# Optimization experiments

Hardware: AMD Instinct MI355X
Metric: run time of the kernel (lower is better)

## Reference

```python
import jax, jax.numpy as jnp
import numpy as np

N = 8192      # number of graph nodes
C = 256       # feature_size
D = C // 2    # projection dim


def setup_inputs() -> dict:
    key = jax.random.key(0)
    ks = jax.random.split(key, 10)
    s_in = 1.0 / np.sqrt(C + 3)   # torch Linear default init scale (uniform bound)
    s_r = 1.0 / np.sqrt(D)
    return {
        "landmarks": jax.random.normal(ks[0], (1, N, 3), dtype=jnp.float32),
        "features": jax.random.normal(ks[1], (1, N, C), dtype=jnp.float32),
        # weights stored [in, out]
        "Wi": jax.random.uniform(ks[2], (C + 3, D), jnp.float32, -s_in, s_in),
        "bi": jax.random.uniform(ks[3], (D,), jnp.float32, -s_in, s_in),
        "Wj": jax.random.uniform(ks[4], (C + 3, D), jnp.float32, -s_in, s_in),
        "bj": jax.random.uniform(ks[5], (D,), jnp.float32, -s_in, s_in),
        "Wk": jax.random.uniform(ks[6], (C + 3, D), jnp.float32, -s_in, s_in),
        "bk": jax.random.uniform(ks[7], (D,), jnp.float32, -s_in, s_in),
        "Wr": jax.random.uniform(ks[8], (D, C), jnp.float32, -s_r, s_r),
        "br": jax.random.uniform(ks[9], (C,), jnp.float32, -s_r, s_r),
    }


def reference(landmarks, features, Wi, bi, Wj, bj, Wk, bk, Wr, br):
    # concat coords + features, drop the singleton batch dim: [N, C+3]
    x = jnp.concatenate([landmarks, features], axis=2)[0]
    fi = x @ Wi + bi                       # [N, D]
    fj = x @ Wj + bj                       # [N, D]
    fk = x @ Wk + bk                       # [N, D]
    att = jax.nn.sigmoid(fi @ fj.T)        # [N, N] sigmoid scores (non-softmax)
    att = att / jnp.sum(att, axis=1, keepdims=True)  # row-sum normalize
    out = (att @ fk) @ Wr + br             # [N, C] restored
    return features + out[None]            # residual, back to [1, N, C]
```

## Files before the change

kernel.cpp:

```cpp
#include <hip/hip_runtime.h>
#include <stdint.h>

#define N_NODES 8192
#define KPAD 272
#define OUTC 384

typedef __attribute__((ext_vector_type(8))) short bhalf8;
typedef __attribute__((ext_vector_type(16))) float f32x16;
typedef __attribute__((ext_vector_type(4))) float f32x4;

__device__ inline unsigned short f2bf_rne(float f) {
    unsigned u = __builtin_bit_cast(unsigned, f);
    u += 0x7FFFu + ((u >> 16) & 1u);
    return (unsigned short)(u >> 16);
}

__device__ inline float bf2f(unsigned short u) {
    return __builtin_bit_cast(float, ((unsigned)u) << 16);
}

__device__ inline bhalf8 mk8(unsigned a, unsigned b, unsigned c, unsigned d) {
    union { unsigned u[4]; bhalf8 v; } U;
    U.u[0] = a; U.u[1] = b; U.u[2] = c; U.u[3] = d;
    return U.v;
}

#define GLD_TO_LDS(gptr, lptr)                                                              \
    __builtin_amdgcn_global_load_lds((const __attribute__((address_space(1))) void*)(gptr), \
                                     (__attribute__((address_space(3))) void*)(lptr), 16, 0, 0)

__global__ void k_prep(const float* __restrict__ landmarks, const float* __restrict__ features,
                       const float* __restrict__ Wi, const float* __restrict__ bi,
                       const float* __restrict__ Wj, const float* __restrict__ bj,
                       const float* __restrict__ Wk, const float* __restrict__ bk,
                       const float* __restrict__ Wr,
                       unsigned short* __restrict__ xb, unsigned short* __restrict__ WcatT,
                       unsigned short* __restrict__ WrT, float* __restrict__ bcat) {
    int idx = blockIdx.x * 256 + threadIdx.x;
    const int XB_N = N_NODES * KPAD;
    const int WC_N = OUTC * KPAD;
    const int WR_N = 256 * 128;
    if (idx < XB_N) {
        int i = idx / KPAD, kk = idx - i * KPAD;
        float v = 0.f;
        if (kk < 256) v = features[i * 256 + kk];
        else if (kk < 259) v = landmarks[i * 3 + (kk - 256)];
        xb[idx] = f2bf_rne(v);
        return;
    }
    idx -= XB_N;
    if (idx < WC_N) {
        int n = idx / KPAD, kk = idx - n * KPAD;
        int sel = n >> 7, d = n & 127;
        const float* W = (sel == 0) ? Wi : ((sel == 1) ? Wj : Wk);
        float v = 0.f;
        if (kk < 256) v = W[(kk + 3) * 128 + d];
        else if (kk < 259) v = W[(kk - 256) * 128 + d];
        WcatT[idx] = f2bf_rne(v);
        return;
    }
    idx -= WC_N;
    if (idx < WR_N) {
        int c = idx >> 7, d = idx & 127;
        WrT[idx] = f2bf_rne(Wr[d * 256 + c]);
        return;
    }
    idx -= WR_N;
    if (idx < OUTC) {
        float v = (idx < 128) ? bi[idx] : ((idx < 256) ? bj[idx - 128] : bk[idx - 256]);
        bcat[idx] = v;
    }
}

__global__ __launch_bounds__(256) void k_proj(const unsigned short* __restrict__ xb,
                                              const unsigned short* __restrict__ WcatT,
                                              const float* __restrict__ bcat,
                                              unsigned short* __restrict__ fi,
                                              unsigned short* __restrict__ fj,
                                              unsigned short* __restrict__ fkT) {
    const int tid = threadIdx.x;
    const int w = tid >> 6, l = tid & 63, h = l >> 5, ln = l & 31;
    const int i0 = blockIdx.x * 32;
    f32x16 acc[3] = {};
#pragma unroll
    for (int s = 0; s < 17; ++s) {
        bhalf8 a = *(const bhalf8*)(xb + (size_t)(i0 + ln) * KPAD + s * 16 + h * 8);
#pragma unroll
        for (int t = 0; t < 3; ++t) {
            int n = 96 * w + 32 * t + ln;
            bhalf8 b = *(const bhalf8*)(WcatT + (size_t)n * KPAD + s * 16 + h * 8);
            acc[t] = __builtin_amdgcn_mfma_f32_32x32x16_bf16(a, b, acc[t], 0, 0, 0);
        }
    }
#pragma unroll
    for (int t = 0; t < 3; ++t) {
        int n = 96 * w + 32 * t + ln;
        int sel = n >> 7, d = n & 127;
        float bias = bcat[n];
#pragma unroll
        for (int q = 0; q < 4; ++q) {
            int ib = i0 + 8 * q + 4 * h;
            if (sel < 2) {
                unsigned short* dst = sel ? fj : fi;
#pragma unroll
                for (int r = 0; r < 4; ++r)
                    dst[(size_t)(ib + r) * 128 + d] = f2bf_rne(acc[t][4 * q + r] + bias);
            } else {
                ushort4 pk;
                pk.x = f2bf_rne(acc[t][4 * q + 0] + bias);
                pk.y = f2bf_rne(acc[t][4 * q + 1] + bias);
                pk.z = f2bf_rne(acc[t][4 * q + 2] + bias);
                pk.w = f2bf_rne(acc[t][4 * q + 3] + bias);
                *(ushort4*)(fkT + (size_t)d * N_NODES + ib) = pk;
            }
        }
    }
}

__global__ __launch_bounds__(256, 2) void k_attn(const unsigned short* __restrict__ fi,
                                                 const unsigned short* __restrict__ fj,
                                                 const unsigned short* __restrict__ fkT,
                                                 unsigned short* __restrict__ num_part,
                                                 float* __restrict__ den_part) {
    __shared__ __align__(16) char smem[66560];
    float* bufA = (float*)smem;
    float* bufB = (float*)(smem + 17408);
    float* denb = (float*)(smem + 65536);

    const int tid = threadIdx.x;
    const int w = tid >> 6, l = tid & 63, h = l >> 5, ln = l & 31;
    const int jq = blockIdx.x & 3, rt = blockIdx.x >> 2;
    const int i0 = rt * 64;
    const int jbase = jq * 2048;

    bhalf8 bfi[2][8];
#pragma unroll
    for (int nt = 0; nt < 2; ++nt)
#pragma unroll
        for (int s = 0; s < 8; ++s)
            bfi[nt][s] = *(const bhalf8*)(fi + (size_t)(i0 + nt * 32 + ln) * 128 + s * 16 + h * 8);

    f32x16 acc[8] = {};
    float dacc0 = 0.f, dacc1 = 0.f;

    const int rsub = l >> 4;
    const int cph = l & 15;

    {
        const int j00 = jbase + ((rt & 15) * 128);
#pragma unroll
        for (int q = 0; q < 8; ++q) {
            int r = w * 32 + q * 4 + rsub;
            int c = cph ^ (r & 15);
            GLD_TO_LDS(fkT + (size_t)r * N_NODES + j00 + c * 8, smem + (w * 32 + q * 4) * 256);
        }
    }

    for (int mt = 0; mt < 16; ++mt) {
        __syncthreads();
        char* fk_cur = smem + ((mt & 1) ? 32768 : 0);
        char* fk_nxt = smem + ((mt & 1) ? 0 : 32768);
        if (mt < 15) {
            const int j0n = jbase + (((mt + 1 + rt) & 15) * 128);
#pragma unroll
            for (int q = 0; q < 8; ++q) {
                int r = w * 32 + q * 4 + rsub;
                int c = cph ^ (r & 15);
                GLD_TO_LDS(fkT + (size_t)r * N_NODES + j0n + c * 8, fk_nxt + (w * 32 + q * 4) * 256);
            }
        }
        const int j0 = jbase + (((mt + rt) & 15) * 128);

        f32x16 st0 = {}, st1 = {};
        const int jrow = j0 + w * 32 + ln;
#pragma unroll
        for (int s = 0; s < 8; ++s) {
            bhalf8 af = *(const bhalf8*)(fj + (size_t)jrow * 128 + s * 16 + h * 8);
            st0 = __builtin_amdgcn_mfma_f32_32x32x16_bf16(af, bfi[0][s], st0, 0, 0, 0);
            st1 = __builtin_amdgcn_mfma_f32_32x32x16_bf16(af, bfi[1][s], st1, 0, 0, 0);
        }

        float sv0[16], sv1[16];
#pragma unroll
        for (int r = 0; r < 16; ++r) {
            float x0 = __builtin_amdgcn_rcpf(1.f + __builtin_amdgcn_exp2f(st0[r] * -1.44269504f));
            float x1 = __builtin_amdgcn_rcpf(1.f + __builtin_amdgcn_exp2f(st1[r] * -1.44269504f));
            dacc0 += x0; dacc1 += x1;
            sv0[r] = x0; sv1[r] = x1;
        }
        unsigned p0[8], p1[8], x0v[8], x1v[8];
#pragma unroll
        for (int q = 0; q < 8; ++q) {
            p0[q] = __builtin_amdgcn_perm(__builtin_bit_cast(unsigned, sv0[2 * q + 1]),
                                          __builtin_bit_cast(unsigned, sv0[2 * q]), 0x07060302u);
            p1[q] = __builtin_amdgcn_perm(__builtin_bit_cast(unsigned, sv1[2 * q + 1]),
                                          __builtin_bit_cast(unsigned, sv1[2 * q]), 0x07060302u);
        }
#pragma unroll
        for (int q = 0; q < 8; ++q) {
            x0v[q] = (unsigned)__shfl_xor((int)p0[q], 32, 64);
            x1v[q] = (unsigned)__shfl_xor((int)p1[q], 32, 64);
        }
        bhalf8 fb[2][2];
        if (h == 0) {
            fb[0][0] = mk8(p0[0], p0[1], x0v[0], x0v[1]);
            fb[0][1] = mk8(p0[4], p0[5], x0v[4], x0v[5]);
            fb[1][0] = mk8(p1[0], p1[1], x1v[0], x1v[1]);
            fb[1][1] = mk8(p1[4], p1[5], x1v[4], x1v[5]);
        } else {
            fb[0][0] = mk8(x0v[2], x0v[3], p0[2], p0[3]);
            fb[0][1] = mk8(x0v[6], x0v[7], p0[6], p0[7]);
            fb[1][0] = mk8(x1v[2], x1v[3], p1[2], p1[3]);
            fb[1][1] = mk8(x1v[6], x1v[7], p1[6], p1[7]);
        }
#pragma unroll
        for (int m4 = 0; m4 < 4; ++m4) {
#pragma unroll
            for (int s2 = 0; s2 < 2; ++s2) {
                int row = m4 * 32 + ln;
                int c = (w * 4 + s2 * 2 + h) ^ (row & 15);
                bhalf8 af = *(const bhalf8*)(fk_cur + row * 256 + c * 16);
                acc[m4 * 2 + 0] = __builtin_amdgcn_mfma_f32_32x32x16_bf16(af, fb[0][s2], acc[m4 * 2 + 0], 0, 0, 0);
                acc[m4 * 2 + 1] = __builtin_amdgcn_mfma_f32_32x32x16_bf16(af, fb[1][s2], acc[m4 * 2 + 1], 0, 0, 0);
            }
        }
    }

    {
        float o0 = __shfl_xor(dacc0, 32, 64);
        float o1 = __shfl_xor(dacc1, 32, 64);
        dacc0 += o0; dacc1 += o1;
    }
    if (h == 0) {
        denb[w * 64 + ln] = dacc0;
        denb[w * 64 + 32 + ln] = dacc1;
    }

#pragma unroll
    for (int half = 0; half < 2; ++half) {
        __syncthreads();
        if (w < 2) {
            float* buf = w ? bufB : bufA;
#pragma unroll
            for (int m2 = 0; m2 < 2; ++m2) {
                int m4 = half * 2 + m2;
#pragma unroll
                for (int nt = 0; nt < 2; ++nt) {
                    int iloc = nt * 32 + ln;
#pragma unroll
                    for (int q = 0; q < 4; ++q) {
                        int d = m2 * 32 + 8 * q + 4 * h;
                        f32x4 v = {acc[m4 * 2 + nt][4 * q + 0], acc[m4 * 2 + nt][4 * q + 1],
                                   acc[m4 * 2 + nt][4 * q + 2], acc[m4 * 2 + nt][4 * q + 3]};
                        *(f32x4*)(buf + iloc * 68 + d) = v;
                    }
                }
            }
        }
        __syncthreads();
        if (w >= 2) {
            float* buf = (w == 3) ? bufB : bufA;
#pragma unroll
            for (int m2 = 0; m2 < 2; ++m2) {
                int m4 = half * 2 + m2;
#pragma unroll
                for (int nt = 0; nt < 2; ++nt) {
                    int iloc = nt * 32 + ln;
#pragma unroll
                    for (int q = 0; q < 4; ++q) {
                        int d = m2 * 32 + 8 * q + 4 * h;
                        f32x4 old = *(f32x4*)(buf + iloc * 68 + d);
                        f32x4 v = {acc[m4 * 2 + nt][4 * q + 0], acc[m4 * 2 + nt][4 * q + 1],
                                   acc[m4 * 2 + nt][4 * q + 2], acc[m4 * 2 + nt][4 * q + 3]};
                        *(f32x4*)(buf + iloc * 68 + d) = old + v;
                    }
                }
            }
        }
        __syncthreads();
#pragma unroll
        for (int e = 0; e < 4; ++e) {
            int v = e * 256 + tid;
            int iloc = v >> 4;
            int d4 = (v & 15) * 4;
            f32x4 s = *(f32x4*)(bufA + iloc * 68 + d4) + *(f32x4*)(bufB + iloc * 68 + d4);
            ushort4 pk;
            pk.x = f2bf_rne(s.x); pk.y = f2bf_rne(s.y);
            pk.z = f2bf_rne(s.z); pk.w = f2bf_rne(s.w);
            *(ushort4*)(num_part + (size_t)(jq * N_NODES + i0 + iloc) * 128 + half * 64 + d4) = pk;
        }
    }
    __syncthreads();
    if (tid < 64) {
        den_part[(size_t)jq * N_NODES + i0 + tid] =
            denb[tid] + denb[64 + tid] + denb[128 + tid] + denb[192 + tid];
    }
}

__global__ __launch_bounds__(256) void k_out(const unsigned short* __restrict__ num_part,
                                             const float* __restrict__ den_part,
                                             const unsigned short* __restrict__ WrT,
                                             const float* __restrict__ br,
                                             const float* __restrict__ features,
                                             float* __restrict__ out) {
    __shared__ __align__(16) char smem[73728];
    unsigned short* t_s = (unsigned short*)(smem + 65536);
    const int tid = threadIdx.x, w = tid >> 6, l = tid & 63, h = l >> 5, ln = l & 31;
    const int i0 = blockIdx.x * 32;
    {
        int rsub = l >> 4, cph = l & 15;
#pragma unroll
        for (int q = 0; q < 16; ++q) {
            int r = w * 64 + q * 4 + rsub;
            int c = cph ^ (r & 15);
            GLD_TO_LDS(WrT + (size_t)r * 128 + c * 8, (char*)smem + (w * 64 + q * 4) * 256);
        }
    }
#pragma unroll
    for (int e = 0; e < 2; ++e) {
        int v = e * 256 + tid;
        int r = v >> 4, c8 = v & 15;
        float s[8] = {};
        float den = 0.f;
#pragma unroll
        for (int q = 0; q < 4; ++q) {
            const unsigned short* p = num_part + (size_t)(q * N_NODES + i0 + r) * 128 + c8 * 8;
            union { uint4 u; unsigned short us[8]; } U;
            U.u = *(const uint4*)p;
#pragma unroll
            for (int z = 0; z < 8; ++z) s[z] += bf2f(U.us[z]);
            den += den_part[(size_t)q * N_NODES + i0 + r];
        }
        float inv = 1.0f / den;
        union { ushort4 a[2]; uint4 u; } P;
#pragma unroll
        for (int z = 0; z < 8; ++z) ((unsigned short*)&P)[z] = f2bf_rne(s[z] * inv);
        int pc = c8 ^ (r & 15);
        *(uint4*)((char*)t_s + r * 256 + pc * 16) = P.u;
    }
    __syncthreads();
    f32x16 acc[2] = {};
#pragma unroll
    for (int s = 0; s < 8; ++s) {
        int ca = (s * 2 + h) ^ (ln & 15);
        bhalf8 af = *(const bhalf8*)((char*)t_s + ln * 256 + ca * 16);
#pragma unroll
        for (int nt = 0; nt < 2; ++nt) {
            int row = w * 64 + nt * 32 + ln;
            int c = (s * 2 + h) ^ (row & 15);
            bhalf8 bf = *(const bhalf8*)((char*)smem + row * 256 + c * 16);
            acc[nt] = __builtin_amdgcn_mfma_f32_32x32x16_bf16(af, bf, acc[nt], 0, 0, 0);
        }
    }
#pragma unroll
    for (int nt = 0; nt < 2; ++nt) {
        int cc = w * 64 + nt * 32 + ln;
        float bias = br[cc];
#pragma unroll
        for (int q = 0; q < 4; ++q) {
#pragma unroll
            for (int r = 0; r < 4; ++r) {
                int i = i0 + 8 * q + 4 * h + r;
                out[(size_t)i * 256 + cc] = acc[nt][4 * q + r] + bias + features[(size_t)i * 256 + cc];
            }
        }
    }
}

extern "C" void kernel_launch(void* const* d_in, const int* in_sizes, int n_in,
                              void* d_out, int out_size, void* d_ws, size_t ws_size,
                              hipStream_t stream) {
    const float* landmarks = (const float*)d_in[0];
    const float* features  = (const float*)d_in[1];
    const float* Wi = (const float*)d_in[2];
    const float* bi = (const float*)d_in[3];
    const float* Wj = (const float*)d_in[4];
    const float* bj = (const float*)d_in[5];
    const float* Wk = (const float*)d_in[6];
    const float* bk = (const float*)d_in[7];
    const float* Wr = (const float*)d_in[8];
    const float* br = (const float*)d_in[9];

    char* ws = (char*)d_ws;
    unsigned short* xb      = (unsigned short*)(ws + 0);
    unsigned short* WcatT   = (unsigned short*)(ws + 4456448);
    unsigned short* WrT     = (unsigned short*)(ws + 4665344);
    float*          bcat    = (float*)(ws + 4730880);
    unsigned short* fi      = (unsigned short*)(ws + 4732416);
    unsigned short* fjp     = (unsigned short*)(ws + 6829568);
    unsigned short* fkT     = (unsigned short*)(ws + 8926720);
    unsigned short* num_part= (unsigned short*)(ws + 11023872);
    float*          den_part= (float*)(ws + 19412480);

    float* out = (float*)d_out;

    hipLaunchKernelGGL(k_prep, dim3(9242), dim3(256), 0, stream,
                       landmarks, features, Wi, bi, Wj, bj, Wk, bk, Wr, xb, WcatT, WrT, bcat);
    hipLaunchKernelGGL(k_proj, dim3(256), dim3(256), 0, stream, xb, WcatT, bcat, fi, fjp, fkT);
    hipLaunchKernelGGL(k_attn, dim3(512), dim3(256), 0, stream, fi, fjp, fkT, num_part, den_part);
    hipLaunchKernelGGL(k_out, dim3(256), dim3(256), 0, stream, num_part, den_part, WrT, br, features, out);
}
```

Before: 183.2 us.

## Restage attention fi into LDS, prefetch fj into registers, and widen proj/out grids

The attention kernel now stages fi through LDS instead of holding it in registers. It double-buffers the fj rows in registers, prefetching the next tile's fj alongside the fk LDS staging, and unrolls the loop by two tiles so the global fj loads overlap with compute. The projection and output kernels are split across more blocks (three output segments and two channel halves), giving each block less work and the GPU more parallelism. The attention kernel grows its shared memory to 80 KB, which may reduce occupancy, and the extra LDS reads of fi add traffic in exchange for fewer registers held across the loop.

```diff
diff --git a/kernel.cpp b/kernel.cpp
--- a/kernel.cpp
+++ b/kernel.cpp
@@ -23,6 +23,10 @@
     union { unsigned u[4]; bhalf8 v; } U;
     U.u[0] = a; U.u[1] = b; U.u[2] = c; U.u[3] = d;
     return U.v;
+}
+
+__device__ inline float sigm(float s) {
+    return __builtin_amdgcn_rcpf(1.f + __builtin_amdgcn_exp2f(s * -1.44269504f));
 }
 
 #define GLD_TO_LDS(gptr, lptr)                                                              \
@@ -80,39 +84,33 @@
                                               unsigned short* __restrict__ fkT) {
     const int tid = threadIdx.x;
     const int w = tid >> 6, l = tid & 63, h = l >> 5, ln = l & 31;
-    const int i0 = blockIdx.x * 32;
-    f32x16 acc[3] = {};
+    const int rt = blockIdx.x / 3, nseg = blockIdx.x - rt * 3;
+    const int i0 = rt * 32;
+    const int n = nseg * 128 + w * 32 + ln;
+    f32x16 acc = {};
 #pragma unroll
     for (int s = 0; s < 17; ++s) {
         bhalf8 a = *(const bhalf8*)(xb + (size_t)(i0 + ln) * KPAD + s * 16 + h * 8);
-#pragma unroll
-        for (int t = 0; t < 3; ++t) {
-            int n = 96 * w + 32 * t + ln;
-            bhalf8 b = *(const bhalf8*)(WcatT + (size_t)n * KPAD + s * 16 + h * 8);
-            acc[t] = __builtin_amdgcn_mfma_f32_32x32x16_bf16(a, b, acc[t], 0, 0, 0);
-        }
-    }
-#pragma unroll
-    for (int t = 0; t < 3; ++t) {
-        int n = 96 * w + 32 * t + ln;
-        int sel = n >> 7, d = n & 127;
-        float bias = bcat[n];
-#pragma unroll
-        for (int q = 0; q < 4; ++q) {
-            int ib = i0 + 8 * q + 4 * h;
-            if (sel < 2) {
-                unsigned short* dst = sel ? fj : fi;
-#pragma unroll
-                for (int r = 0; r < 4; ++r)
-                    dst[(size_t)(ib + r) * 128 + d] = f2bf_rne(acc[t][4 * q + r] + bias);
-            } else {
-                ushort4 pk;
-                pk.x = f2bf_rne(acc[t][4 * q + 0] + bias);
-                pk.y = f2bf_rne(acc[t][4 * q + 1] + bias);
-                pk.z = f2bf_rne(acc[t][4 * q + 2] + bias);
-                pk.w = f2bf_rne(acc[t][4 * q + 3] + bias);
-                *(ushort4*)(fkT + (size_t)d * N_NODES + ib) = pk;
-            }
+        bhalf8 b = *(const bhalf8*)(WcatT + (size_t)n * KPAD + s * 16 + h * 8);
+        acc = __builtin_amdgcn_mfma_f32_32x32x16_bf16(a, b, acc, 0, 0, 0);
+    }
+    const int d = n & 127;
+    const float bias = bcat[n];
+#pragma unroll
+    for (int q = 0; q < 4; ++q) {
+        int ib = i0 + 8 * q + 4 * h;
+        if (nseg < 2) {
+            unsigned short* dst = nseg ? fj : fi;
+#pragma unroll
+            for (int r = 0; r < 4; ++r)
+                dst[(size_t)(ib + r) * 128 + d] = f2bf_rne(acc[4 * q + r] + bias);
+        } else {
+            ushort4 pk;
+            pk.x = f2bf_rne(acc[4 * q + 0] + bias);
+            pk.y = f2bf_rne(acc[4 * q + 1] + bias);
+            pk.z = f2bf_rne(acc[4 * q + 2] + bias);
+            pk.w = f2bf_rne(acc[4 * q + 3] + bias);
+            *(ushort4*)(fkT + (size_t)d * N_NODES + ib) = pk;
         }
     }
 }
@@ -122,10 +120,13 @@
                                                  const unsigned short* __restrict__ fkT,
                                                  unsigned short* __restrict__ num_part,
                                                  float* __restrict__ den_part) {
-    __shared__ __align__(16) char smem[66560];
-    float* bufA = (float*)smem;
-    float* bufB = (float*)(smem + 17408);
-    float* denb = (float*)(smem + 65536);
+    __shared__ __align__(16) char smem[81920];
+    char* fi_s = smem;
+    char* fk0 = smem + 16384;
+    char* fk1 = smem + 49152;
+    float* bufA = (float*)(smem + 16384);
+    float* bufB = (float*)(smem + 33792);
+    float* denb = (float*)smem;
 
     const int tid = threadIdx.x;
     const int w = tid >> 6, l = tid & 63, h = l >> 5, ln = l & 31;
@@ -133,68 +134,60 @@
     const int i0 = rt * 64;
     const int jbase = jq * 2048;
 
-    bhalf8 bfi[2][8];
-#pragma unroll
-    for (int nt = 0; nt < 2; ++nt)
-#pragma unroll
-        for (int s = 0; s < 8; ++s)
-            bfi[nt][s] = *(const bhalf8*)(fi + (size_t)(i0 + nt * 32 + ln) * 128 + s * 16 + h * 8);
+    const int rsub = l >> 4;
+    const int cph = l & 15;
 
     f32x16 acc[8] = {};
     float dacc0 = 0.f, dacc1 = 0.f;
 
-    const int rsub = l >> 4;
-    const int cph = l & 15;
-
+#pragma unroll
+    for (int q = 0; q < 4; ++q) {
+        int r = w * 16 + q * 4 + rsub;
+        int c = cph ^ (r & 15);
+        GLD_TO_LDS(fi + (size_t)(i0 + r) * 128 + c * 8, fi_s + (w * 16 + q * 4) * 256);
+    }
     {
         const int j00 = jbase + ((rt & 15) * 128);
 #pragma unroll
         for (int q = 0; q < 8; ++q) {
             int r = w * 32 + q * 4 + rsub;
             int c = cph ^ (r & 15);
-            GLD_TO_LDS(fkT + (size_t)r * N_NODES + j00 + c * 8, smem + (w * 32 + q * 4) * 256);
-        }
-    }
-
-    for (int mt = 0; mt < 16; ++mt) {
-        __syncthreads();
-        char* fk_cur = smem + ((mt & 1) ? 32768 : 0);
-        char* fk_nxt = smem + ((mt & 1) ? 0 : 32768);
-        if (mt < 15) {
-            const int j0n = jbase + (((mt + 1 + rt) & 15) * 128);
-#pragma unroll
-            for (int q = 0; q < 8; ++q) {
-                int r = w * 32 + q * 4 + rsub;
-                int c = cph ^ (r & 15);
-                GLD_TO_LDS(fkT + (size_t)r * N_NODES + j0n + c * 8, fk_nxt + (w * 32 + q * 4) * 256);
-            }
-        }
-        const int j0 = jbase + (((mt + rt) & 15) * 128);
-
+            GLD_TO_LDS(fkT + (size_t)r * N_NODES + j00 + c * 8, fk0 + (w * 32 + q * 4) * 256);
+        }
+    }
+    bhalf8 fjA[8], fjB[8];
+    {
+        const int jrow = jbase + ((rt & 15) * 128) + w * 32 + ln;
+#pragma unroll
+        for (int s = 0; s < 8; ++s)
+            fjA[s] = *(const bhalf8*)(fj + (size_t)jrow * 128 + s * 16 + h * 8);
+    }
+
+    auto compute_tile = [&](bhalf8 (&fjr)[8], char* fk_cur) {
         f32x16 st0 = {}, st1 = {};
-        const int jrow = j0 + w * 32 + ln;
+        const int rm = ln & 15;
 #pragma unroll
         for (int s = 0; s < 8; ++s) {
-            bhalf8 af = *(const bhalf8*)(fj + (size_t)jrow * 128 + s * 16 + h * 8);
-            st0 = __builtin_amdgcn_mfma_f32_32x32x16_bf16(af, bfi[0][s], st0, 0, 0, 0);
-            st1 = __builtin_amdgcn_mfma_f32_32x32x16_bf16(af, bfi[1][s], st1, 0, 0, 0);
-        }
-
-        float sv0[16], sv1[16];
-#pragma unroll
-        for (int r = 0; r < 16; ++r) {
-            float x0 = __builtin_amdgcn_rcpf(1.f + __builtin_amdgcn_exp2f(st0[r] * -1.44269504f));
-            float x1 = __builtin_amdgcn_rcpf(1.f + __builtin_amdgcn_exp2f(st1[r] * -1.44269504f));
-            dacc0 += x0; dacc1 += x1;
-            sv0[r] = x0; sv1[r] = x1;
+            int c = (s * 2 + h) ^ rm;
+            bhalf8 b0 = *(const bhalf8*)(fi_s + ln * 256 + c * 16);
+            bhalf8 b1 = *(const bhalf8*)(fi_s + (32 + ln) * 256 + c * 16);
+            st0 = __builtin_amdgcn_mfma_f32_32x32x16_bf16(fjr[s], b0, st0, 0, 0, 0);
+            st1 = __builtin_amdgcn_mfma_f32_32x32x16_bf16(fjr[s], b1, st1, 0, 0, 0);
         }
         unsigned p0[8], p1[8], x0v[8], x1v[8];
 #pragma unroll
         for (int q = 0; q < 8; ++q) {
-            p0[q] = __builtin_amdgcn_perm(__builtin_bit_cast(unsigned, sv0[2 * q + 1]),
-                                          __builtin_bit_cast(unsigned, sv0[2 * q]), 0x07060302u);
-            p1[q] = __builtin_amdgcn_perm(__builtin_bit_cast(unsigned, sv1[2 * q + 1]),
-                                          __builtin_bit_cast(unsigned, sv1[2 * q]), 0x07060302u);
+            float a0 = sigm(st0[2 * q]), b0 = sigm(st0[2 * q + 1]);
+            dacc0 += a0 + b0;
+            p0[q] = __builtin_amdgcn_perm(__builtin_bit_cast(unsigned, b0),
+                                          __builtin_bit_cast(unsigned, a0), 0x07060302u);
+        }
+#pragma unroll
+        for (int q = 0; q < 8; ++q) {
+            float a1 = sigm(st1[2 * q]), b1 = sigm(st1[2 * q + 1]);
+            dacc1 += a1 + b1;
+            p1[q] = __builtin_amdgcn_perm(__builtin_bit_cast(unsigned, b1),
+                                          __builtin_bit_cast(unsigned, a1), 0x07060302u);
         }
 #pragma unroll
         for (int q = 0; q < 8; ++q) {
@@ -224,7 +217,39 @@
                 acc[m4 * 2 + 1] = __builtin_amdgcn_mfma_f32_32x32x16_bf16(af, fb[1][s2], acc[m4 * 2 + 1], 0, 0, 0);
             }
         }
-    }
+    };
+
+    auto stage_fk = [&](int t, char* dst) {
+        const int j0 = jbase + (((t + rt) & 15) * 128);
+#pragma unroll
+        for (int q = 0; q < 8; ++q) {
+            int r = w * 32 + q * 4 + rsub;
+            int c = cph ^ (r & 15);
+            GLD_TO_LDS(fkT + (size_t)r * N_NODES + j0 + c * 8, dst + (w * 32 + q * 4) * 256);
+        }
+    };
+    auto load_fj = [&](int t, bhalf8 (&dst)[8]) {
+        const int jrow = jbase + (((t + rt) & 15) * 128) + w * 32 + ln;
+#pragma unroll
+        for (int s = 0; s < 8; ++s)
+            dst[s] = *(const bhalf8*)(fj + (size_t)jrow * 128 + s * 16 + h * 8);
+    };
+
+    for (int tr = 0; tr < 8; ++tr) {
+        const int t0 = 2 * tr;
+        __syncthreads();
+        stage_fk(t0 + 1, fk1);
+        load_fj(t0 + 1, fjB);
+        compute_tile(fjA, fk0);
+        __syncthreads();
+        if (tr < 7) {
+            stage_fk(t0 + 2, fk0);
+            load_fj(t0 + 2, fjA);
+        }
+        compute_tile(fjB, fk1);
+    }
+
+    __syncthreads();
 
     {
         float o0 = __shfl_xor(dacc0, 32, 64);
@@ -303,17 +328,18 @@
                                              const float* __restrict__ br,
                                              const float* __restrict__ features,
                                              float* __restrict__ out) {
-    __shared__ __align__(16) char smem[73728];
-    unsigned short* t_s = (unsigned short*)(smem + 65536);
+    __shared__ __align__(16) char smem[40960];
+    unsigned short* t_s = (unsigned short*)(smem + 32768);
     const int tid = threadIdx.x, w = tid >> 6, l = tid & 63, h = l >> 5, ln = l & 31;
-    const int i0 = blockIdx.x * 32;
+    const int i0 = (blockIdx.x >> 1) * 32;
+    const int ch = blockIdx.x & 1;
     {
         int rsub = l >> 4, cph = l & 15;
 #pragma unroll
-        for (int q = 0; q < 16; ++q) {
-            int r = w * 64 + q * 4 + rsub;
+        for (int q = 0; q < 8; ++q) {
+            int r = w * 32 + q * 4 + rsub;
             int c = cph ^ (r & 15);
-            GLD_TO_LDS(WrT + (size_t)r * 128 + c * 8, (char*)smem + (w * 64 + q * 4) * 256);
+            GLD_TO_LDS(WrT + (size_t)(ch * 128 + r) * 128 + c * 8, smem + (w * 32 + q * 4) * 256);
         }
     }
 #pragma unroll
@@ -339,29 +365,25 @@
         *(uint4*)((char*)t_s + r * 256 + pc * 16) = P.u;
     }
     __syncthreads();
-    f32x16 acc[2] = {};
+    f32x16 acc = {};
 #pragma unroll
     for (int s = 0; s < 8; ++s) {
         int ca = (s * 2 + h) ^ (ln & 15);
         bhalf8 af = *(const bhalf8*)((char*)t_s + ln * 256 + ca * 16);
-#pragma unroll
-        for (int nt = 0; nt < 2; ++nt) {
-            int row = w * 64 + nt * 32 + ln;
-            int c = (s * 2 + h) ^ (row & 15);
-            bhalf8 bf = *(const bhalf8*)((char*)smem + row * 256 + c * 16);
-            acc[nt] = __builtin_amdgcn_mfma_f32_32x32x16_bf16(af, bf, acc[nt], 0, 0, 0);
-        }
-    }
-#pragma unroll
-    for (int nt = 0; nt < 2; ++nt) {
-        int cc = w * 64 + nt * 32 + ln;
+        int row = w * 32 + ln;
+        int c = (s * 2 + h) ^ (row & 15);
+        bhalf8 bf = *(const bhalf8*)(smem + row * 256 + c * 16);
+        acc = __builtin_amdgcn_mfma_f32_32x32x16_bf16(af, bf, acc, 0, 0, 0);
+    }
+    {
+        int cc = ch * 128 + w * 32 + ln;
         float bias = br[cc];
 #pragma unroll
         for (int q = 0; q < 4; ++q) {
 #pragma unroll
             for (int r = 0; r < 4; ++r) {
                 int i = i0 + 8 * q + 4 * h + r;
-                out[(size_t)i * 256 + cc] = acc[nt][4 * q + r] + bias + features[(size_t)i * 256 + cc];
+                out[(size_t)i * 256 + cc] = acc[4 * q + r] + bias + features[(size_t)i * 256 + cc];
             }
         }
     }
@@ -396,7 +418,7 @@
 
     hipLaunchKernelGGL(k_prep, dim3(9242), dim3(256), 0, stream,
                        landmarks, features, Wi, bi, Wj, bj, Wk, bk, Wr, xb, WcatT, WrT, bcat);
-    hipLaunchKernelGGL(k_proj, dim3(256), dim3(256), 0, stream, xb, WcatT, bcat, fi, fjp, fkT);
+    hipLaunchKernelGGL(k_proj, dim3(768), dim3(256), 0, stream, xb, WcatT, bcat, fi, fjp, fkT);
     hipLaunchKernelGGL(k_attn, dim3(512), dim3(256), 0, stream, fi, fjp, fkT, num_part, den_part);
-    hipLaunchKernelGGL(k_out, dim3(256), dim3(256), 0, stream, num_part, den_part, WrT, br, features, out);
-}
+    hipLaunchKernelGGL(k_out, dim3(512), dim3(256), 0, stream, num_part, den_part, WrT, br, features, out);
+}
```

New measurement: 221.1 us. 20.7% more time.
